# Kernel tuning notes

Hardware: AMD Instinct MI355X
Metric: run time of the kernel (lower is better)

The kernel has to match this reference:

```python
import jax, jax.numpy as jnp
import numpy as np

N_NODES = 50000
N_EDGES = 800000
HEADS = 4
NEG_SLOPE = 0.2  # PyG GATConv default leaky_relu slope
EPS = 1e-16      # PyG softmax denominator epsilon


def setup_inputs() -> dict:
    key = jax.random.key(0)
    ks = jax.random.split(key, 20)
    g = lambda k, shape, s=0.1: jax.random.normal(k, shape, dtype=jnp.float32) * s
    inp = {
        "x": g(ks[0], (N_NODES, 7), 1.0),
        "edge_index": jax.random.randint(ks[1], (2, N_EDGES), 0, N_NODES, dtype=jnp.int32),
        # encoder MLP 7 -> 64 -> 64
        "enc_w1": g(ks[2], (7, 64)), "enc_b1": jnp.zeros((64,), jnp.float32),
        "enc_w2": g(ks[3], (64, 64)), "enc_b2": jnp.zeros((64,), jnp.float32),
        # GATConv 1: in=64, heads=4, out_per_head=64, concat -> 256
        "g1_w": g(ks[4], (64, HEADS * 64)),
        "g1_as": g(ks[5], (HEADS, 64)), "g1_ad": g(ks[6], (HEADS, 64)),
        "g1_b": jnp.zeros((HEADS * 64,), jnp.float32),
        # GATConv 2: in=256, heads=4, out_per_head=16, concat -> 64
        "g2_w": g(ks[7], (256, HEADS * 16)),
        "g2_as": g(ks[8], (HEADS, 16)), "g2_ad": g(ks[9], (HEADS, 16)),
        "g2_b": jnp.zeros((HEADS * 16,), jnp.float32),
        # decoder MLP 64 -> 64 -> 4
        "dec_w1": g(ks[10], (64, 64)), "dec_b1": jnp.zeros((64,), jnp.float32),
        "dec_w2": g(ks[11], (64, 4)), "dec_b2": jnp.zeros((4,), jnp.float32),
    }
    return inp


def gat_conv(x, src, dst, n_nodes, W, a_src, a_dst, bias):
    """PyG GATConv (concat=True, self-loops already appended to src/dst)."""
    H, C = a_src.shape
    h = (x @ W).reshape(n_nodes, H, C)                      # [N,H,C]
    alpha_src = jnp.einsum('nhc,hc->nh', h, a_src)          # [N,H]
    alpha_dst = jnp.einsum('nhc,hc->nh', h, a_dst)          # [N,H]
    e = jax.nn.leaky_relu(alpha_src[src] + alpha_dst[dst], NEG_SLOPE)  # [E,H]
    # segment softmax over each destination node's incoming edges
    m = jax.ops.segment_max(e, dst, num_segments=n_nodes)   # [N,H]
    e = jnp.exp(e - m[dst])
    denom = jax.ops.segment_sum(e, dst, num_segments=n_nodes)
    alpha = e / (denom[dst] + EPS)                          # [E,H]
    msg = h[src] * alpha[:, :, None]                        # [E,H,C]
    out = jax.ops.segment_sum(msg, dst, num_segments=n_nodes)  # [N,H,C]
    return out.reshape(n_nodes, H * C) + bias


def reference(x, edge_index, enc_w1, enc_b1, enc_w2, enc_b2,
              g1_w, g1_as, g1_ad, g1_b, g2_w, g2_as, g2_ad, g2_b,
              dec_w1, dec_b1, dec_w2, dec_b2):
    n = x.shape[0]
    loop = jnp.arange(n, dtype=edge_index.dtype)
    src = jnp.concatenate([edge_index[0], loop])  # add self loops (PyG default)
    dst = jnp.concatenate([edge_index[1], loop])

    h = jax.nn.relu(x @ enc_w1 + enc_b1) @ enc_w2 + enc_b2   # encoder
    h = gat_conv(h, src, dst, n, g1_w, g1_as, g1_ad, g1_b)   # GAT layer 1
    h = jax.nn.elu(h)                                        # activation (dropout off in eval)
    h = gat_conv(h, src, dst, n, g2_w, g2_as, g2_ad, g2_b)   # GAT layer 2 (last: no act)
    out = jax.nn.relu(h @ dec_w1 + dec_b1) @ dec_w2 + dec_b2  # decoder
    return out
```

## Files before the change

### kernel.cpp

```cpp
#include <hip/hip_runtime.h>
#include <hip/hip_bf16.h>

#define N_NODES 50000
#define N_EDGES 800000
#define ET_EDGES 850000
#define HEADS 4
#define ENC_BLOCKS 1563

#define BSHIFT 8
#define NBUK 196
#define BCAP 6144
#define EB_PER_BLOCK 4096
#define EB_BLOCKS 208

#define G12NB 782
#define NAGG_BLOCKS 3125

#define W1HI 0
#define W1LO 16384
#define W2HI 32768
#define W2LO 49152
#define GCHI 65536
#define GCLO 69632
#define WT_TOTAL 73728

typedef __attribute__((ext_vector_type(8))) short bf16x8;
typedef __attribute__((ext_vector_type(4))) float f32x4;
#define MFMA16(a, b, c) __builtin_amdgcn_mfma_f32_16x16x32_bf16((a), (b), (c), 0, 0, 0)

__device__ __forceinline__ float lrelu(float v) { return v > 0.f ? v : 0.2f * v; }

__device__ __forceinline__ unsigned short f2bf(float f) {
    unsigned int u = __float_as_uint(f);
    u = (u + 0x7FFFu + ((u >> 16) & 1u)) >> 16;
    return (unsigned short)u;
}
__device__ __forceinline__ float bf2f(unsigned short h) {
    return __uint_as_float((unsigned int)h << 16);
}

__device__ __forceinline__ void edge_sd(const int* __restrict__ ei, int e, int& s, int& d) {
    if (e < N_EDGES) { s = ei[e]; d = ei[N_EDGES + e]; }
    else { s = d = e - N_EDGES; }
}

__global__ __launch_bounds__(256) void zerofold_kernel(
    int* __restrict__ bcur,
    const float* __restrict__ g1w, const float* __restrict__ g1as, const float* __restrict__ g1ad,
    float* __restrict__ wsf, float* __restrict__ wdf,
    const float* __restrict__ g2w, const float* __restrict__ g2as, const float* __restrict__ g2ad,
    unsigned short* __restrict__ wtb) {
    int b = blockIdx.x;
    int tid = threadIdx.x;
    if (b == 0) {
        if (tid < NBUK) bcur[tid] = 0;
        return;
    }
    if (b == 1) {
        int h = tid >> 6, k = tid & 63;
        float as_acc = 0.f, ad_acc = 0.f;
        #pragma unroll 8
        for (int c = 0; c < 64; ++c) {
            float w = g1w[k * 256 + h * 64 + c];
            as_acc += w * g1as[h * 64 + c];
            ad_acc += w * g1ad[h * 64 + c];
        }
        wsf[tid] = as_acc;
        wdf[tid] = ad_acc;
        return;
    }
    if (b < 18) {
        int gidx0 = (b - 2) * 2048 + tid * 8;
        #pragma unroll
        for (int u = 0; u < 8; ++u) {
            int idx = gidx0 + u;
            float w;
            int dst;
            if (idx < 16384) {
                int h = idx >> 12, q = (idx >> 6) & 63, k = idx & 63;
                w = g1w[k * 256 + h * 64 + q];
                dst = W1HI + idx;
            } else {
                int i2 = idx - 16384;
                int c = i2 >> 8, K = i2 & 255;
                w = g2w[K * 64 + c];
                dst = W2HI + i2;
            }
            unsigned short hi = f2bf(w);
            unsigned short lo = f2bf(w - bf2f(hi));
            wtb[dst] = hi;
            wtb[dst + 16384] = lo;
        }
        return;
    }
    {
        int gidx0 = (b - 18) * 2048 + tid * 8;
        #pragma unroll
        for (int u = 0; u < 8; ++u) {
            int idx = gidx0 + u;
            int j = idx >> 8, K = idx & 255;
            float acc = 0.f;
            if (j < 8) {
                int h = j >> 1;
                const float* gv = (j & 1) ? g2ad : g2as;
                #pragma unroll
                for (int cc = 0; cc < 16; ++cc)
                    acc += g2w[K * 64 + h * 16 + cc] * gv[h * 16 + cc];
            }
            unsigned short hi = f2bf(acc);
            unsigned short lo = f2bf(acc - bf2f(hi));
            wtb[GCHI + idx] = hi;
            wtb[GCLO + idx] = lo;
        }
        return;
    }
}

__global__ __launch_bounds__(256) void mega_kernel(
    const int* __restrict__ ei, int* __restrict__ bcur, int* __restrict__ ebuf,
    const float* __restrict__ x, const float* __restrict__ w1, const float* __restrict__ b1,
    const float* __restrict__ w2, const float* __restrict__ b2,
    const float* __restrict__ wsf, const float* __restrict__ wdf,
    unsigned short* __restrict__ henc, float* __restrict__ as1, float* __restrict__ ad1) {
    __shared__ union {
        struct { int es[EB_PER_BLOCK]; int ed[EB_PER_BLOCK]; int h[NBUK]; int base[NBUK]; } buk;
        struct { float w2[4096]; float t[32][64]; float xx[32][8]; float he[32][65]; float wf[8 * 65]; } enc;
    } u;
    int tid = threadIdx.x;
    if (blockIdx.x < EB_BLOCKS) {
        for (int i = tid; i < NBUK; i += 256) u.buk.h[i] = 0;
        int e0 = blockIdx.x * EB_PER_BLOCK;
        __syncthreads();
        #pragma unroll
        for (int r = 0; r < EB_PER_BLOCK / 256; ++r) {
            int i = r * 256 + tid;
            int e = e0 + i;
            if (e < ET_EDGES) {
                int s, d; edge_sd(ei, e, s, d);
                u.buk.es[i] = s;
                u.buk.ed[i] = d;
                atomicAdd(&u.buk.h[d >> BSHIFT], 1);
            } else {
                u.buk.ed[i] = -1;
            }
        }
        __syncthreads();
        for (int i = tid; i < NBUK; i += 256) {
            int c = u.buk.h[i];
            u.buk.base[i] = c ? atomicAdd(bcur + i, c) : 0;
            u.buk.h[i] = 0;
        }
        __syncthreads();
        #pragma unroll
        for (int r = 0; r < EB_PER_BLOCK / 256; ++r) {
            int i = r * 256 + tid;
            int d = u.buk.ed[i];
            if (d >= 0) {
                int b = d >> BSHIFT;
                int off = atomicAdd(&u.buk.h[b], 1);
                ebuf[b * BCAP + u.buk.base[b] + off] = ((d & 255) << 16) | u.buk.es[i];
            }
        }
        return;
    }
    int node0 = (blockIdx.x - EB_BLOCKS) * 32;
    for (int i = tid; i < 4096; i += 256) u.enc.w2[i] = w2[i];
    for (int i = tid; i < 224; i += 256) {
        int src = node0 * 7 + i;
        u.enc.xx[i / 7][i % 7] = (src < N_NODES * 7) ? x[src] : 0.f;
    }
    for (int i = tid; i < 512; i += 256) {
        int g = i >> 6, k = i & 63;
        int h = g & 3;
        u.enc.wf[g * 65 + k] = (g < 4) ? wsf[h * 64 + k] : wdf[h * 64 + k];
    }
    int c = tid & 63;
    int mg = tid >> 6;
    float w1c[7];
    #pragma unroll
    for (int k = 0; k < 7; ++k) w1c[k] = w1[k * 64 + c];
    float b1c = b1[c];
    __syncthreads();
    #pragma unroll
    for (int m = 0; m < 8; ++m) {
        int nn = mg * 8 + m;
        float a = b1c;
        #pragma unroll
        for (int k = 0; k < 7; ++k) a += u.enc.xx[nn][k] * w1c[k];
        u.enc.t[nn][c] = fmaxf(a, 0.f);
    }
    __syncthreads();
    float acc[8];
    float b2c = b2[c];
    #pragma unroll
    for (int m = 0; m < 8; ++m) acc[m] = b2c;
    #pragma unroll 4
    for (int k = 0; k < 64; ++k) {
        float w = u.enc.w2[k * 64 + c];
        #pragma unroll
        for (int m = 0; m < 8; ++m) acc[m] += u.enc.t[mg * 8 + m][k] * w;
    }
    #pragma unroll
    for (int m = 0; m < 8; ++m) {
        int nn = mg * 8 + m;
        int node = node0 + nn;
        u.enc.he[nn][c] = acc[m];
        if (node < N_NODES) henc[node * 64 + c] = f2bf(acc[m]);
    }
    __syncthreads();
    {
        int nn = tid >> 3, r = tid & 7;
        int node = node0 + nn;
        const float* wf = u.enc.wf + r * 65;
        float sum = 0.f;
        #pragma unroll 8
        for (int k = 0; k < 64; ++k) sum += u.enc.he[nn][k] * wf[k];
        if (node < N_NODES) {
            int hh = r & 3;
            if (r < 4) as1[node * 4 + hh] = sum;
            else       ad1[node * 4 + hh] = sum;
        }
    }
}

__global__ __launch_bounds__(256) void bucket_csr_kernel(
    const int* __restrict__ ebuf, const int* __restrict__ bcur,
    int* __restrict__ rowbeg, int* __restrict__ degarr, int* __restrict__ csr_src) {
    __shared__ int s_deg[256];
    __shared__ int s_cur[256];
    __shared__ int s_w[4];
    int b = blockIdx.x;
    int tid = threadIdx.x;
    s_deg[tid] = 0;
    int cnt = bcur[b];
    int base = b * BCAP;
    const int* eb = ebuf + base;
    int node0 = b << BSHIFT;
    __syncthreads();
    for (int i = tid; i < cnt; i += 256) atomicAdd(&s_deg[eb[i] >> 16], 1);
    __syncthreads();
    int v = s_deg[tid];
    int lane = tid & 63, w = tid >> 6;
    int xv = v;
    #pragma unroll
    for (int off = 1; off < 64; off <<= 1) {
        int t = __shfl_up(xv, off);
        if (lane >= off) xv += t;
    }
    if (lane == 63) s_w[w] = xv;
    __syncthreads();
    if (tid == 0) {
        int a = 0;
        #pragma unroll
        for (int j = 0; j < 4; ++j) { int t = s_w[j]; s_w[j] = a; a += t; }
    }
    __syncthreads();
    int excl = xv - v + s_w[w];
    s_cur[tid] = excl;
    int node = node0 + tid;
    if (node < N_NODES) {
        rowbeg[node] = base + excl;
        degarr[node] = v;
    }
    __syncthreads();
    for (int i = tid; i < cnt; i += 256) {
        int p = eb[i];
        int pos = atomicAdd(&s_cur[p >> 16], 1);
        csr_src[base + pos] = p & 0xFFFF;
    }
}

__global__ __launch_bounds__(256) void aggregate1_kernel(
    const int* __restrict__ rowbeg, const int* __restrict__ degarr, const int* __restrict__ csr_src,
    const float* __restrict__ as, const float* __restrict__ ad,
    const unsigned short* __restrict__ henc, unsigned short* __restrict__ agg) {
    __shared__ int    ls[16][17];
    __shared__ float4 lp[16][17];
    int tid = threadIdx.x;
    int gg = tid >> 4, lane16 = tid & 15;
    int n = blockIdx.x * 16 + gg;
    if (n >= N_NODES) return;
    int base = rowbeg[n];
    int deg  = degarr[n];
    float4 add = *(const float4*)(ad + n * 4);

    float4 l = make_float4(0.f, 0.f, 0.f, 0.f);
    float acc[4][4];
    #pragma unroll
    for (int f = 0; f < 4; ++f)
        #pragma unroll
        for (int h = 0; h < 4; ++h) acc[f][h] = 0.f;

    for (int c0 = 0; c0 < deg; c0 += 16) {
        int j = c0 + lane16;
        int s = 0;
        float4 p = make_float4(0.f, 0.f, 0.f, 0.f);
        if (j < deg) {
            s = csr_src[base + j];
            float4 a = *(const float4*)(as + s * 4);
            p.x = __expf(lrelu(a.x + add.x));
            p.y = __expf(lrelu(a.y + add.y));
            p.z = __expf(lrelu(a.z + add.z));
            p.w = __expf(lrelu(a.w + add.w));
            l.x += p.x; l.y += p.y; l.z += p.z; l.w += p.w;
        }
        ls[gg][lane16] = s;
        lp[gg][lane16] = p;
        int cnt = min(16, deg - c0);
        const int*    lsw = ls[gg];
        const float4* lpw = lp[gg];
        int e = 0;
        for (; e + 4 <= cnt; e += 4) {
            ushort4 r0 = *(const ushort4*)(henc + lsw[e+0] * 64 + lane16 * 4);
            ushort4 r1 = *(const ushort4*)(henc + lsw[e+1] * 64 + lane16 * 4);
            ushort4 r2 = *(const ushort4*)(henc + lsw[e+2] * 64 + lane16 * 4);
            ushort4 r3 = *(const ushort4*)(henc + lsw[e+3] * 64 + lane16 * 4);
            float4 p0 = lpw[e+0], p1 = lpw[e+1], p2 = lpw[e+2], p3 = lpw[e+3];
            #define ACC1(r, pp) { \
                float v0 = bf2f(r.x), v1 = bf2f(r.y), v2 = bf2f(r.z), v3 = bf2f(r.w); \
                acc[0][0] += v0*pp.x; acc[0][1] += v0*pp.y; acc[0][2] += v0*pp.z; acc[0][3] += v0*pp.w; \
                acc[1][0] += v1*pp.x; acc[1][1] += v1*pp.y; acc[1][2] += v1*pp.z; acc[1][3] += v1*pp.w; \
                acc[2][0] += v2*pp.x; acc[2][1] += v2*pp.y; acc[2][2] += v2*pp.z; acc[2][3] += v2*pp.w; \
                acc[3][0] += v3*pp.x; acc[3][1] += v3*pp.y; acc[3][2] += v3*pp.z; acc[3][3] += v3*pp.w; }
            ACC1(r0, p0) ACC1(r1, p1) ACC1(r2, p2) ACC1(r3, p3)
        }
        for (; e < cnt; ++e) {
            ushort4 r = *(const ushort4*)(henc + lsw[e] * 64 + lane16 * 4);
            float4 pp = lpw[e];
            ACC1(r, pp)
        }
    }
    #pragma unroll
    for (int off = 1; off < 16; off <<= 1) {
        l.x += __shfl_xor(l.x, off);
        l.y += __shfl_xor(l.y, off);
        l.z += __shfl_xor(l.z, off);
        l.w += __shfl_xor(l.w, off);
    }
    float inv[4];
    inv[0] = 1.f / (l.x + 1e-16f);
    inv[1] = 1.f / (l.y + 1e-16f);
    inv[2] = 1.f / (l.z + 1e-16f);
    inv[3] = 1.f / (l.w + 1e-16f);
    const size_t PL = (size_t)N_NODES * 64;
    #pragma unroll
    for (int h = 0; h < 4; ++h) {
        ushort4 o;
        o.x = f2bf(acc[0][h] * inv[h]);
        o.y = f2bf(acc[1][h] * inv[h]);
        o.z = f2bf(acc[2][h] * inv[h]);
        o.w = f2bf(acc[3][h] * inv[h]);
        *(ushort4*)(agg + h * PL + (size_t)n * 64 + lane16 * 4) = o;
    }
}

__global__ __launch_bounds__(256, 1) void gemm12_kernel(
    const unsigned short* __restrict__ agg, const unsigned short* __restrict__ wtb,
    const float* __restrict__ g1b, unsigned short* __restrict__ h2,
    float* __restrict__ as2, float* __restrict__ ad2) {
    __shared__ unsigned short sw[40960];
    __shared__ unsigned short s1[16384];
    int tid = threadIdx.x;
    int node0 = blockIdx.x * 64;
    int lane = tid & 63, w = tid >> 6;
    int lrow = lane & 15, g = lane >> 4;
    const size_t PL = (size_t)N_NODES * 64;

    {
        const uint4* src = (const uint4*)(wtb + W1HI);
        uint4* dst = (uint4*)sw;
        #pragma unroll
        for (int r = 0; r < 16; ++r) {
            int i = r * 256 + tid;
            dst[i ^ ((i >> 3) & 7)] = src[i];
        }
    }
    int arow = node0 + w * 16 + lrow;
    if (arow >= N_NODES) arow = N_NODES - 1;
    bf16x8 aF[4][2];
    #pragma unroll
    for (int h = 0; h < 4; ++h)
        #pragma unroll
        for (int ks = 0; ks < 2; ++ks)
            aF[h][ks] = *(const bf16x8*)(agg + (size_t)h * PL + (size_t)arow * 64 + ks * 32 + g * 8);
    float bb[4][4];
    #pragma unroll
    for (int h = 0; h < 4; ++h)
        #pragma unroll
        for (int qt = 0; qt < 4; ++qt)
            bb[h][qt] = g1b[h * 64 + qt * 16 + lrow];
    __syncthreads();

    f32x4 acc1[4][4];
    #pragma unroll
    for (int h = 0; h < 4; ++h)
        #pragma unroll
        for (int qt = 0; qt < 4; ++qt) acc1[h][qt] = (f32x4){0.f, 0.f, 0.f, 0.f};
    #pragma unroll
    for (int h = 0; h < 4; ++h) {
        #pragma unroll
        for (int ks = 0; ks < 2; ++ks) {
            #pragma unroll
            for (int qt = 0; qt < 4; ++qt) {
                int q = qt * 16 + lrow;
                int byt = (h * 8192 + q * 128 + ks * 64 + g * 16) ^ ((q & 7) << 4);
                bf16x8 bH = *(const bf16x8*)((char*)sw + byt);
                bf16x8 bL = *(const bf16x8*)((char*)sw + byt + 32768);
                acc1[h][qt] = MFMA16(aF[h][ks], bH, acc1[h][qt]);
                acc1[h][qt] = MFMA16(aF[h][ks], bL, acc1[h][qt]);
            }
        }
    }
    #pragma unroll
    for (int h = 0; h < 4; ++h) {
        #pragma unroll
        for (int qt = 0; qt < 4; ++qt) {
            int col = h * 64 + qt * 16 + lrow;
            #pragma unroll
            for (int i = 0; i < 4; ++i) {
                int r = w * 16 + g * 4 + i;
                float t = acc1[h][qt][i] + bb[h][qt];
                t = t > 0.f ? t : (__expf(t) - 1.f);
                int byt = (r * 512 + col * 2) ^ ((r & 7) << 4);
                *(unsigned short*)((char*)s1 + byt) = f2bf(t);
            }
        }
    }
    __syncthreads();
    {
        const uint4* src = (const uint4*)(wtb + W2HI);
        uint4* dst = (uint4*)sw;
        #pragma unroll
        for (int r = 0; r < 20; ++r) {
            int i = r * 256 + tid;
            dst[i ^ ((i >> 5) & 7)] = src[i];
        }
    }
    __syncthreads();
    f32x4 acc2[4];
    f32x4 accg = (f32x4){0.f, 0.f, 0.f, 0.f};
    #pragma unroll
    for (int qt = 0; qt < 4; ++qt) acc2[qt] = (f32x4){0.f, 0.f, 0.f, 0.f};
    int rloc = w * 16 + lrow;
    int rx = (rloc & 7) << 4;
    #pragma unroll
    for (int ks = 0; ks < 8; ++ks) {
        int kb = ks * 64 + g * 16;
        bf16x8 aF2 = *(const bf16x8*)((char*)s1 + ((rloc * 512 + kb) ^ rx));
        #pragma unroll
        for (int qt = 0; qt < 4; ++qt) {
            int c = qt * 16 + lrow;
            int byt = (c * 512 + kb) ^ ((c & 7) << 4);
            bf16x8 bH = *(const bf16x8*)((char*)sw + byt);
            bf16x8 bL = *(const bf16x8*)((char*)sw + byt + 32768);
            acc2[qt] = MFMA16(aF2, bH, acc2[qt]);
            acc2[qt] = MFMA16(aF2, bL, acc2[qt]);
        }
        {
            int byt = 65536 + ((lrow * 512 + kb) ^ ((lrow & 7) << 4));
            bf16x8 gH = *(const bf16x8*)((char*)sw + byt);
            bf16x8 gL = *(const bf16x8*)((char*)sw + byt + 8192);
            accg = MFMA16(aF2, gH, accg);
            accg = MFMA16(aF2, gL, accg);
        }
    }
    #pragma unroll
    for (int i = 0; i < 4; ++i) {
        int node = node0 + w * 16 + g * 4 + i;
        if (node < N_NODES) {
            #pragma unroll
            for (int qt = 0; qt < 4; ++qt)
                h2[(size_t)node * 64 + qt * 16 + lrow] = f2bf(acc2[qt][i]);
            if (lrow < 8) {
                float v = accg[i];
                int hh = lrow >> 1;
                if (lrow & 1) ad2[node * 4 + hh] = v;
                else          as2[node * 4 + hh] = v;
            }
        }
    }
}

__global__ __launch_bounds__(256) void aggregate2_kernel(
    const int* __restrict__ rowbeg, const int* __restrict__ degarr, const int* __restrict__ csr_src,
    const float* __restrict__ as, const float* __restrict__ ad,
    const unsigned short* __restrict__ h, float* __restrict__ out) {
    __shared__ int    ls[16][17];
    __shared__ float4 lp[16][17];
    int tid = threadIdx.x;
    int gg = tid >> 4, lane16 = tid & 15;
    int n = blockIdx.x * 16 + gg;
    if (n >= N_NODES) return;
    int base = rowbeg[n];
    int deg  = degarr[n];
    int head = lane16 >> 2;
    float4 add = *(const float4*)(ad + n * 4);

    float4 l = make_float4(0.f, 0.f, 0.f, 0.f);
    float acc[4];
    acc[0] = acc[1] = acc[2] = acc[3] = 0.f;

    for (int c0 = 0; c0 < deg; c0 += 16) {
        int j = c0 + lane16;
        int s = 0;
        float4 p = make_float4(0.f, 0.f, 0.f, 0.f);
        if (j < deg) {
            s = csr_src[base + j];
            float4 a = *(const float4*)(as + s * 4);
            p.x = __expf(lrelu(a.x + add.x));
            p.y = __expf(lrelu(a.y + add.y));
            p.z = __expf(lrelu(a.z + add.z));
            p.w = __expf(lrelu(a.w + add.w));
            l.x += p.x; l.y += p.y; l.z += p.z; l.w += p.w;
        }
        ls[gg][lane16] = s;
        lp[gg][lane16] = p;
        int cnt = min(16, deg - c0);
        const int*   lsw = ls[gg];
        const float* lpf = (const float*)lp[gg];
        int e = 0;
        for (; e + 4 <= cnt; e += 4) {
            ushort4 r0 = *(const ushort4*)(h + lsw[e+0] * 64 + lane16 * 4);
            ushort4 r1 = *(const ushort4*)(h + lsw[e+1] * 64 + lane16 * 4);
            ushort4 r2 = *(const ushort4*)(h + lsw[e+2] * 64 + lane16 * 4);
            ushort4 r3 = *(const ushort4*)(h + lsw[e+3] * 64 + lane16 * 4);
            float p0 = lpf[(e+0) * 4 + head];
            float p1 = lpf[(e+1) * 4 + head];
            float p2 = lpf[(e+2) * 4 + head];
            float p3 = lpf[(e+3) * 4 + head];
            acc[0] += bf2f(r0.x)*p0 + bf2f(r1.x)*p1 + bf2f(r2.x)*p2 + bf2f(r3.x)*p3;
            acc[1] += bf2f(r0.y)*p0 + bf2f(r1.y)*p1 + bf2f(r2.y)*p2 + bf2f(r3.y)*p3;
            acc[2] += bf2f(r0.z)*p0 + bf2f(r1.z)*p1 + bf2f(r2.z)*p2 + bf2f(r3.z)*p3;
            acc[3] += bf2f(r0.w)*p0 + bf2f(r1.w)*p1 + bf2f(r2.w)*p2 + bf2f(r3.w)*p3;
        }
        for (; e < cnt; ++e) {
            ushort4 r = *(const ushort4*)(h + lsw[e] * 64 + lane16 * 4);
            float pe = lpf[e * 4 + head];
            acc[0] += bf2f(r.x) * pe;
            acc[1] += bf2f(r.y) * pe;
            acc[2] += bf2f(r.z) * pe;
            acc[3] += bf2f(r.w) * pe;
        }
    }
    #pragma unroll
    for (int off = 1; off < 16; off <<= 1) {
        l.x += __shfl_xor(l.x, off);
        l.y += __shfl_xor(l.y, off);
        l.z += __shfl_xor(l.z, off);
        l.w += __shfl_xor(l.w, off);
    }
    float lh = (head == 0) ? l.x : (head == 1) ? l.y : (head == 2) ? l.z : l.w;
    float inv = 1.f / (lh + 1e-16f);
    float4 o;
    o.x = acc[0] * inv; o.y = acc[1] * inv; o.z = acc[2] * inv; o.w = acc[3] * inv;
    *(float4*)(out + (size_t)n * 64 + lane16 * 4) = o;
}

__global__ __launch_bounds__(256) void decoder32_kernel(
    const float* __restrict__ hin, const float* __restrict__ gb,
    const float* __restrict__ w1, const float* __restrict__ b1,
    const float* __restrict__ w2, const float* __restrict__ b2, float* __restrict__ out) {
    __shared__ float s_w1[4096];
    __shared__ float s_w2[256];
    __shared__ float s_h[32][64];
    __shared__ float s_t[32][64];
    int tid = threadIdx.x;
    int node0 = blockIdx.x * 32;
    for (int i = tid; i < 4096; i += 256) s_w1[i] = w1[i];
    if (tid < 256) s_w2[tid] = w2[tid];
    for (int i = tid; i < 2048; i += 256) {
        int nn = i >> 6, k = i & 63;
        int node = node0 + nn;
        s_h[nn][k] = (node < N_NODES ? hin[(size_t)node * 64 + k] : 0.f) + gb[k];
    }
    __syncthreads();
    int c = tid & 63;
    int mg = tid >> 6;
    float b1c = b1[c];
    float acc[8];
    #pragma unroll
    for (int m = 0; m < 8; ++m) acc[m] = b1c;
    #pragma unroll 4
    for (int k = 0; k < 64; ++k) {
        float w = s_w1[k * 64 + c];
        #pragma unroll
        for (int m = 0; m < 8; ++m) acc[m] += s_h[mg * 8 + m][k] * w;
    }
    #pragma unroll
    for (int m = 0; m < 8; ++m) s_t[mg * 8 + m][c] = fmaxf(acc[m], 0.f);
    __syncthreads();
    if (tid < 128) {
        int m = tid >> 2, j = tid & 3;
        int node = node0 + m;
        if (node < N_NODES) {
            float a = b2[j];
            #pragma unroll 16
            for (int k = 0; k < 64; ++k) a += s_t[m][k] * s_w2[k * 4 + j];
            out[node * 4 + j] = a;
        }
    }
}

extern "C" void kernel_launch(void* const* d_in, const int* in_sizes, int n_in,
                              void* d_out, int out_size, void* d_ws, size_t ws_size,
                              hipStream_t stream) {
    const float* x      = (const float*)d_in[0];
    const int*   ei     = (const int*)d_in[1];
    const float* enc_w1 = (const float*)d_in[2];
    const float* enc_b1 = (const float*)d_in[3];
    const float* enc_w2 = (const float*)d_in[4];
    const float* enc_b2 = (const float*)d_in[5];
    const float* g1_w   = (const float*)d_in[6];
    const float* g1_as  = (const float*)d_in[7];
    const float* g1_ad  = (const float*)d_in[8];
    const float* g1_b   = (const float*)d_in[9];
    const float* g2_w   = (const float*)d_in[10];
    const float* g2_as  = (const float*)d_in[11];
    const float* g2_ad  = (const float*)d_in[12];
    const float* g2_b   = (const float*)d_in[13];
    const float* dec_w1 = (const float*)d_in[14];
    const float* dec_b1 = (const float*)d_in[15];
    const float* dec_w2 = (const float*)d_in[16];
    const float* dec_b2 = (const float*)d_in[17];

    const int N = N_NODES;

    float* ws   = (float*)d_ws;
    unsigned short* henc = (unsigned short*)ws;
    unsigned short* wtb  = (unsigned short*)(ws + 1700000);
    unsigned short* agg  = (unsigned short*)(ws + 3200000);
    unsigned short* h2   = (unsigned short*)(ws + 16000000);
    float* out2 = ws + 19200000;
    unsigned short* out1 = (unsigned short*)(ws + 22400000);
    float* as1  = ws + 35200000;
    float* ad1  = as1 + 200000;
    float* as2  = ad1 + 200000;
    float* ad2  = as2 + 200000;
    float* wsf  = ad2 + 200000;
    float* wdf  = wsf + 256;
    int*   ebuf = (int*)out1;
    int*   ib      = (int*)(ws + 36001024);
    int*   bcur    = ib;
    int*   rowbeg  = ib + 256;
    int*   degarr  = ib + 50432;
    int*   csr_src = ib + 100608;

    zerofold_kernel<<<20, 256, 0, stream>>>(bcur, g1_w, g1_as, g1_ad, wsf, wdf,
                                            g2_w, g2_as, g2_ad, wtb);
    mega_kernel<<<EB_BLOCKS + ENC_BLOCKS, 256, 0, stream>>>(
        ei, bcur, ebuf, x, enc_w1, enc_b1, enc_w2, enc_b2, wsf, wdf, henc, as1, ad1);
    bucket_csr_kernel<<<NBUK, 256, 0, stream>>>(ebuf, bcur, rowbeg, degarr, csr_src);

    aggregate1_kernel<<<NAGG_BLOCKS, 256, 0, stream>>>(rowbeg, degarr, csr_src, as1, ad1, henc, agg);
    gemm12_kernel<<<G12NB, 256, 0, stream>>>(agg, wtb, g1_b, h2, as2, ad2);

    aggregate2_kernel<<<NAGG_BLOCKS, 256, 0, stream>>>(rowbeg, degarr, csr_src, as2, ad2, h2, out2);

    decoder32_kernel<<<(N + 31) / 32, 256, 0, stream>>>(out2, g2_b, dec_w1, dec_b1, dec_w2, dec_b2, (float*)d_out);
}
```

Baseline: 245.8 us.

## Split gemm12 work across 8 waves and prefetch layer-2 weights into registers

Doubles the gemm12 block to 512 threads, so each wave handles half the heads in the first GEMM and half the output columns in the second. The attention-coefficient GEMM now runs only on the first four waves. The layer-2 weight tile is loaded from global memory into registers at the start and written to shared memory after the first phase, hiding that load's latency behind the layer-1 compute. The cost is more register pressure and some waves idling during the attention-coefficient step.

Result: slower. 259.5 us (+5.5%).

```diff
diff --git a/kernel.cpp b/kernel.cpp
--- a/kernel.cpp
+++ b/kernel.cpp
@@ -354,7 +354,7 @@
     }
 }
 
-__global__ __launch_bounds__(256, 1) void gemm12_kernel(
+__global__ __launch_bounds__(512, 1) void gemm12_kernel(
     const unsigned short* __restrict__ agg, const unsigned short* __restrict__ wtb,
     const float* __restrict__ g1b, unsigned short* __restrict__ h2,
     float* __restrict__ as2, float* __restrict__ ad2) {
@@ -364,40 +364,48 @@
     int node0 = blockIdx.x * 64;
     int lane = tid & 63, w = tid >> 6;
     int lrow = lane & 15, g = lane >> 4;
+    int rw = w & 3, hp = w >> 2;
     const size_t PL = (size_t)N_NODES * 64;
 
     {
         const uint4* src = (const uint4*)(wtb + W1HI);
         uint4* dst = (uint4*)sw;
         #pragma unroll
-        for (int r = 0; r < 16; ++r) {
-            int i = r * 256 + tid;
+        for (int r = 0; r < 8; ++r) {
+            int i = r * 512 + tid;
             dst[i ^ ((i >> 3) & 7)] = src[i];
         }
     }
-    int arow = node0 + w * 16 + lrow;
+    uint4 w2r[10];
+    {
+        const uint4* src = (const uint4*)(wtb + W2HI);
+        #pragma unroll
+        for (int r = 0; r < 10; ++r) w2r[r] = src[r * 512 + tid];
+    }
+    int arow = node0 + rw * 16 + lrow;
     if (arow >= N_NODES) arow = N_NODES - 1;
-    bf16x8 aF[4][2];
-    #pragma unroll
-    for (int h = 0; h < 4; ++h)
+    bf16x8 aF[2][2];
+    #pragma unroll
+    for (int hh = 0; hh < 2; ++hh)
         #pragma unroll
         for (int ks = 0; ks < 2; ++ks)
-            aF[h][ks] = *(const bf16x8*)(agg + (size_t)h * PL + (size_t)arow * 64 + ks * 32 + g * 8);
-    float bb[4][4];
-    #pragma unroll
-    for (int h = 0; h < 4; ++h)
+            aF[hh][ks] = *(const bf16x8*)(agg + (size_t)(hp * 2 + hh) * PL + (size_t)arow * 64 + ks * 32 + g * 8);
+    float bb[2][4];
+    #pragma unroll
+    for (int hh = 0; hh < 2; ++hh)
         #pragma unroll
         for (int qt = 0; qt < 4; ++qt)
-            bb[h][qt] = g1b[h * 64 + qt * 16 + lrow];
-    __syncthreads();
-
-    f32x4 acc1[4][4];
-    #pragma unroll
-    for (int h = 0; h < 4; ++h)
-        #pragma unroll
-        for (int qt = 0; qt < 4; ++qt) acc1[h][qt] = (f32x4){0.f, 0.f, 0.f, 0.f};
-    #pragma unroll
-    for (int h = 0; h < 4; ++h) {
+            bb[hh][qt] = g1b[(hp * 2 + hh) * 64 + qt * 16 + lrow];
+    __syncthreads();
+
+    f32x4 acc1[2][4];
+    #pragma unroll
+    for (int hh = 0; hh < 2; ++hh)
+        #pragma unroll
+        for (int qt = 0; qt < 4; ++qt) acc1[hh][qt] = (f32x4){0.f, 0.f, 0.f, 0.f};
+    #pragma unroll
+    for (int hh = 0; hh < 2; ++hh) {
+        int h = hp * 2 + hh;
         #pragma unroll
         for (int ks = 0; ks < 2; ++ks) {
             #pragma unroll
@@ -406,20 +414,21 @@
                 int byt = (h * 8192 + q * 128 + ks * 64 + g * 16) ^ ((q & 7) << 4);
                 bf16x8 bH = *(const bf16x8*)((char*)sw + byt);
                 bf16x8 bL = *(const bf16x8*)((char*)sw + byt + 32768);
-                acc1[h][qt] = MFMA16(aF[h][ks], bH, acc1[h][qt]);
-                acc1[h][qt] = MFMA16(aF[h][ks], bL, acc1[h][qt]);
+                acc1[hh][qt] = MFMA16(aF[hh][ks], bH, acc1[hh][qt]);
+                acc1[hh][qt] = MFMA16(aF[hh][ks], bL, acc1[hh][qt]);
             }
         }
     }
     #pragma unroll
-    for (int h = 0; h < 4; ++h) {
+    for (int hh = 0; hh < 2; ++hh) {
+        int h = hp * 2 + hh;
         #pragma unroll
         for (int qt = 0; qt < 4; ++qt) {
             int col = h * 64 + qt * 16 + lrow;
             #pragma unroll
             for (int i = 0; i < 4; ++i) {
-                int r = w * 16 + g * 4 + i;
-                float t = acc1[h][qt][i] + bb[h][qt];
+                int r = rw * 16 + g * 4 + i;
+                float t = acc1[hh][qt][i] + bb[hh][qt];
                 t = t > 0.f ? t : (__expf(t) - 1.f);
                 int byt = (r * 512 + col * 2) ^ ((r & 7) << 4);
                 *(unsigned short*)((char*)s1 + byt) = f2bf(t);
@@ -428,35 +437,34 @@
     }
     __syncthreads();
     {
-        const uint4* src = (const uint4*)(wtb + W2HI);
         uint4* dst = (uint4*)sw;
         #pragma unroll
-        for (int r = 0; r < 20; ++r) {
-            int i = r * 256 + tid;
-            dst[i ^ ((i >> 5) & 7)] = src[i];
-        }
-    }
-    __syncthreads();
-    f32x4 acc2[4];
+        for (int r = 0; r < 10; ++r) {
+            int i = r * 512 + tid;
+            dst[i ^ ((i >> 5) & 7)] = w2r[r];
+        }
+    }
+    __syncthreads();
+    f32x4 acc2[2];
     f32x4 accg = (f32x4){0.f, 0.f, 0.f, 0.f};
-    #pragma unroll
-    for (int qt = 0; qt < 4; ++qt) acc2[qt] = (f32x4){0.f, 0.f, 0.f, 0.f};
-    int rloc = w * 16 + lrow;
+    acc2[0] = (f32x4){0.f, 0.f, 0.f, 0.f};
+    acc2[1] = (f32x4){0.f, 0.f, 0.f, 0.f};
+    int rloc = rw * 16 + lrow;
     int rx = (rloc & 7) << 4;
     #pragma unroll
     for (int ks = 0; ks < 8; ++ks) {
         int kb = ks * 64 + g * 16;
         bf16x8 aF2 = *(const bf16x8*)((char*)s1 + ((rloc * 512 + kb) ^ rx));
         #pragma unroll
-        for (int qt = 0; qt < 4; ++qt) {
-            int c = qt * 16 + lrow;
+        for (int qt = 0; qt < 2; ++qt) {
+            int c = (hp * 2 + qt) * 16 + lrow;
             int byt = (c * 512 + kb) ^ ((c & 7) << 4);
             bf16x8 bH = *(const bf16x8*)((char*)sw + byt);
             bf16x8 bL = *(const bf16x8*)((char*)sw + byt + 32768);
             acc2[qt] = MFMA16(aF2, bH, acc2[qt]);
             acc2[qt] = MFMA16(aF2, bL, acc2[qt]);
         }
-        {
+        if (hp == 0) {
             int byt = 65536 + ((lrow * 512 + kb) ^ ((lrow & 7) << 4));
             bf16x8 gH = *(const bf16x8*)((char*)sw + byt);
             bf16x8 gL = *(const bf16x8*)((char*)sw + byt + 8192);
@@ -466,12 +474,12 @@
     }
     #pragma unroll
     for (int i = 0; i < 4; ++i) {
-        int node = node0 + w * 16 + g * 4 + i;
+        int node = node0 + rw * 16 + g * 4 + i;
         if (node < N_NODES) {
             #pragma unroll
-            for (int qt = 0; qt < 4; ++qt)
-                h2[(size_t)node * 64 + qt * 16 + lrow] = f2bf(acc2[qt][i]);
-            if (lrow < 8) {
+            for (int qt = 0; qt < 2; ++qt)
+                h2[(size_t)node * 64 + (hp * 2 + qt) * 16 + lrow] = f2bf(acc2[qt][i]);
+            if (hp == 0 && lrow < 8) {
                 float v = accg[i];
                 int hh = lrow >> 1;
                 if (lrow & 1) ad2[node * 4 + hh] = v;
@@ -652,7 +660,7 @@
     bucket_csr_kernel<<<NBUK, 256, 0, stream>>>(ebuf, bcur, rowbeg, degarr, csr_src);
 
     aggregate1_kernel<<<NAGG_BLOCKS, 256, 0, stream>>>(rowbeg, degarr, csr_src, as1, ad1, henc, agg);
-    gemm12_kernel<<<G12NB, 256, 0, stream>>>(agg, wtb, g1_b, h2, as2, ad2);
+    gemm12_kernel<<<G12NB, 512, 0, stream>>>(agg, wtb, g1_b, h2, as2, ad2);
 
     aggregate2_kernel<<<NAGG_BLOCKS, 256, 0, stream>>>(rowbeg, degarr, csr_src, as2, ad2, h2, out2);
 
```
